# Kernel tuning notes

Hardware: AMD Instinct MI355X
Metric: run time of the kernel (lower is better)

Reference implementation:

```python
import jax, jax.numpy as jnp
import numpy as np

B, IN_DIM, HID, PROJ, OUT = 32768, 4097, 2048, 512, 3
FEAT = IN_DIM - 1
EPS = 1e-12  # F.normalize eps


def setup_inputs() -> dict:
    key = jax.random.key(0)
    ks = jax.random.split(key, 16)
    x_feat = jax.random.normal(ks[0], (B, FEAT), dtype=jnp.float32)
    flag = jax.random.randint(ks[1], (B, 1), 0, 2).astype(jnp.float32)
    x = jnp.concatenate([x_feat, flag], axis=1)  # [B, IN_DIM], last col is 0/1 flag

    def lin(k, fan_in, fan_out):
        bound = 1.0 / np.sqrt(fan_in)
        kw, kb = jax.random.split(k)
        W = jax.random.uniform(kw, (fan_in, fan_out), jnp.float32, -bound, bound)
        b = jax.random.uniform(kb, (fan_out,), jnp.float32, -bound, bound)
        return W, b

    W1n, b1n = lin(ks[2], FEAT, HID)
    W2n, b2n = lin(ks[3], HID, PROJ)
    Wcn, bcn = lin(ks[4], PROJ, OUT)
    W1o, b1o = lin(ks[5], FEAT, HID)
    W2o, b2o = lin(ks[6], HID, PROJ)
    Wco, bco = lin(ks[7], PROJ, OUT)
    return {"x": x, "W1n": W1n, "b1n": b1n, "W2n": W2n, "b2n": b2n,
            "Wcn": Wcn, "bcn": bcn, "W1o": W1o, "b1o": b1o, "W2o": W2o,
            "b2o": b2o, "Wco": Wco, "bco": bco}


def _path(feat, W1, b1, W2, b2):
    # Linear -> ReLU -> Dropout(eval: identity) -> Linear
    h = jax.nn.relu(feat @ W1 + b1)
    return h @ W2 + b2  # [B, PROJ]


def reference(x, W1n, b1n, W2n, b2n, Wcn, bcn, W1o, b1o, W2o, b2o, Wco, bco):
    flag = x[:, -1:] > 0.5          # [B,1] bool; 1 -> natural path
    feat = x[:, :-1]                # [B, FEAT]
    # Dense 2-expert compute + select (same math as gather/scatter routing).
    z_nat = _path(feat, W1n, b1n, W2n, b2n)
    z_oth = _path(feat, W1o, b1o, W2o, b2o)
    z = jnp.where(flag, z_nat, z_oth)                      # [B, PROJ]
    logits_nat = jax.nn.relu(z_nat) @ Wcn + bcn
    logits_oth = jax.nn.relu(z_oth) @ Wco + bco
    logits = jnp.where(flag, logits_nat, logits_oth)       # [B, OUT]
    norm = jnp.linalg.norm(z, axis=1, keepdims=True)
    z_normalized = z / jnp.maximum(norm, EPS)
    return (z_normalized, logits)
```

## Files before the change

kernel.cpp:

```cpp
#include <hip/hip_runtime.h>
#include <hip/hip_bf16.h>

typedef __bf16 bf16_t;
typedef __attribute__((ext_vector_type(8))) __bf16 bf16x8;
typedef __attribute__((ext_vector_type(4))) __bf16 bf16x4;
typedef __attribute__((ext_vector_type(4))) float f32x4;

#define NROWS 32768
#define FEAT  4096
#define INDIM 4097
#define HID   2048
#define PROJ  512
#define NPAD  33024
#define MTILES 258
#define SENT  0xFFFFFFFFu

__device__ __forceinline__ void load_lds16(const bf16_t* g, char* s) {
  __builtin_amdgcn_global_load_lds(
      (__attribute__((address_space(1))) void*)(void*)g,
      (__attribute__((address_space(3))) void*)s, 16, 0, 0);
}

__global__ __launch_bounds__(256) void init_kernel(unsigned* __restrict__ perm,
                                                   int* __restrict__ cnt) {
  int i = blockIdx.x * 256 + threadIdx.x;
  if (i < NPAD) perm[i] = SENT;
  if (i < 4) cnt[i] = 0;
}

__global__ __launch_bounds__(256) void count_kernel(const float* __restrict__ x,
                                                    int* __restrict__ cnt) {
  int i = blockIdx.x * 256 + threadIdx.x;
  if (i >= NROWS) return;
  float f = x[(long)i * INDIM + FEAT];
  if (f > 0.5f) atomicAdd(&cnt[0], 1);
}

__global__ __launch_bounds__(256) void scatter_kernel(const float* __restrict__ x,
                                                      unsigned* __restrict__ perm,
                                                      int* __restrict__ cnt) {
  int i = blockIdx.x * 256 + threadIdx.x;
  if (i >= NROWS) return;
  float f = x[(long)i * INDIM + FEAT];
  int g = (f > 0.5f) ? 0 : 1;
  int pos = atomicAdd(&cnt[1 + g], 1);
  int off_oth = ((cnt[0] + 127) >> 7) << 7;
  int q = (g == 0) ? pos : off_oth + pos;
  perm[q] = (unsigned)i;
}

__global__ __launch_bounds__(256) void convert_x_kernel(const float* __restrict__ x,
                                                        bf16_t* __restrict__ xbf) {
  const int lane = threadIdx.x & 63;
  const long wid = ((long)blockIdx.x * 256 + threadIdx.x) >> 6;
  const long chunk = wid * 512;
  const long row = chunk >> 12;
  const long col = chunk & 4095;
  const float* src = x + row * INDIM + col + lane;
  bf16_t* dst = xbf + chunk + lane;
#pragma unroll
  for (int j = 0; j < 8; ++j)
    dst[j * 64] = (bf16_t)src[j * 64];
}

__global__ __launch_bounds__(256) void transpose_convert_kernel(
    const float* __restrict__ W, bf16_t* __restrict__ Wt, int K, int N) {
  __shared__ float tile[32][33];
  const int n0 = blockIdx.x << 5;
  const int k0 = blockIdx.y << 5;
  const int t = threadIdx.x;
  const int r = t >> 3;
  const int c4 = (t & 7) << 2;
  f32x4 v = *(const f32x4*)(W + (long)(k0 + r) * N + n0 + c4);
#pragma unroll
  for (int i = 0; i < 4; ++i) tile[r][c4 + i] = v[i];
  __syncthreads();
  bf16x4 o;
#pragma unroll
  for (int i = 0; i < 4; ++i) o[i] = (bf16_t)tile[c4 + i][r];
  *(bf16x4*)(Wt + (long)(n0 + r) * K + k0 + c4) = o;
}

template <bool GATHER, bool RELU_BF16>
__global__ __launch_bounds__(256) void gemm_kernel(
    const bf16_t* __restrict__ A,
    const bf16_t* __restrict__ BtNat, const bf16_t* __restrict__ BtOth,
    const float* __restrict__ biasNat, const float* __restrict__ biasOth,
    void* __restrict__ Cout,
    const unsigned* __restrict__ perm, const int* __restrict__ cnt,
    const int K, const int N) {
  __shared__ char smem[16384];
  const int tid = threadIdx.x;
  const int tile_m = blockIdx.y;
  const int qbase = tile_m << 7;
  if (perm[qbase] == SENT) return;
  const int n0 = blockIdx.x << 7;
  const int n_nat = cnt[0];
  const int m_tiles_nat = (n_nat + 127) >> 7;
  const bool nat = (tile_m < m_tiles_nat);
  const bf16_t* __restrict__ Bt = nat ? BtNat : BtOth;
  const float* __restrict__ bias = nat ? biasNat : biasOth;

  const int r0 = tid >> 2;
  const int kc = tid & 3;
  long arow0, arow1;
  if (GATHER) {
    unsigned p0 = perm[qbase + r0];
    unsigned p1 = perm[qbase + r0 + 64];
    arow0 = (p0 == SENT) ? 0 : (long)p0;
    arow1 = (p1 == SENT) ? 0 : (long)p1;
  } else {
    arow0 = qbase + r0;
    arow1 = qbase + r0 + 64;
  }
  const bf16_t* srcA0 = A + arow0 * K + (kc << 3);
  const bf16_t* srcA1 = A + arow1 * K + (kc << 3);
  const bf16_t* srcB0 = Bt + (long)(n0 + r0) * K + (kc << 3);
  const bf16_t* srcB1 = Bt + (long)(n0 + r0 + 64) * K + (kc << 3);

  const int wave = tid >> 6;
  const int lane = tid & 63;
  const int quad = lane >> 4;
  const int l16 = lane & 15;
  const int wm = (wave >> 1) << 6;
  const int wn = (wave & 1) << 6;

  char* const Alds = smem;
  char* const Blds = smem + 8192;
  char* const dstA0 = Alds + (wave << 10);
  char* const dstA1 = Alds + 4096 + (wave << 10);
  char* const dstB0 = Blds + (wave << 10);
  char* const dstB1 = Blds + 4096 + (wave << 10);

  f32x4 acc[4][4] = {};

  const int kiters = K >> 5;
  for (int kt = 0; kt < kiters; ++kt) {
    __syncthreads();
    load_lds16(srcA0, dstA0);
    load_lds16(srcA1, dstA1);
    load_lds16(srcB0, dstB0);
    load_lds16(srcB1, dstB1);
    srcA0 += 32; srcA1 += 32; srcB0 += 32; srcB1 += 32;
    __syncthreads();
    bf16x8 af[4], bfr[4];
#pragma unroll
    for (int i = 0; i < 4; ++i)
      af[i] = *(const bf16x8*)(Alds + (((wm + (i << 4) + l16) << 5) + (quad << 3)) * 2);
#pragma unroll
    for (int i = 0; i < 4; ++i)
      bfr[i] = *(const bf16x8*)(Blds + (((wn + (i << 4) + l16) << 5) + (quad << 3)) * 2);
#pragma unroll
    for (int mi = 0; mi < 4; ++mi)
#pragma unroll
      for (int ni = 0; ni < 4; ++ni)
        acc[mi][ni] = __builtin_amdgcn_mfma_f32_16x16x32_bf16(af[mi], bfr[ni], acc[mi][ni], 0, 0, 0);
  }

  float bv[4];
#pragma unroll
  for (int ni = 0; ni < 4; ++ni) bv[ni] = bias[n0 + wn + (ni << 4) + l16];

#pragma unroll
  for (int mi = 0; mi < 4; ++mi) {
#pragma unroll
    for (int ni = 0; ni < 4; ++ni) {
#pragma unroll
      for (int r = 0; r < 4; ++r) {
        const int m = wm + (mi << 4) + (quad << 2) + r;
        const int col = n0 + wn + (ni << 4) + l16;
        float v = acc[mi][ni][r] + bv[ni];
        if (RELU_BF16) {
          v = fmaxf(v, 0.0f);
          ((bf16_t*)Cout)[(long)(qbase + m) * N + col] = (bf16_t)v;
        } else {
          ((float*)Cout)[(long)(qbase + m) * N + col] = v;
        }
      }
    }
  }
}

__global__ __launch_bounds__(256) void epilogue_kernel(
    const float* __restrict__ z,
    const float* __restrict__ Wc0, const float* __restrict__ bc0,
    const float* __restrict__ Wc1, const float* __restrict__ bc1,
    const unsigned* __restrict__ perm, const int* __restrict__ cnt,
    float* __restrict__ out_z, float* __restrict__ out_logits) {
  __shared__ float WcL[2][PROJ * 3];
  for (int i = threadIdx.x; i < PROJ * 3; i += 256) {
    WcL[0][i] = Wc0[i];
    WcL[1][i] = Wc1[i];
  }
  __syncthreads();
  const int wave = threadIdx.x >> 6;
  const int lane = threadIdx.x & 63;
  const int q = blockIdx.x * 4 + wave;
  const unsigned orig = perm[q];
  if (orig == SENT) return;
  const int n_nat = cnt[0];
  const int off_oth = ((n_nat + 127) >> 7) << 7;
  const int g = (q < off_oth) ? 0 : 1;

  float zv[8];
  float ss = 0.f, l0 = 0.f, l1 = 0.f, l2 = 0.f;
#pragma unroll
  for (int i = 0; i < 8; ++i) {
    const int k = i * 64 + lane;
    float v = z[(long)q * PROJ + k];
    zv[i] = v;
    ss += v * v;
    float r = fmaxf(v, 0.f);
    const float* w = &WcL[g][k * 3];
    l0 += r * w[0];
    l1 += r * w[1];
    l2 += r * w[2];
  }
#pragma unroll
  for (int off = 32; off > 0; off >>= 1) {
    ss += __shfl_xor(ss, off);
    l0 += __shfl_xor(l0, off);
    l1 += __shfl_xor(l1, off);
    l2 += __shfl_xor(l2, off);
  }
  const float inv = 1.f / fmaxf(sqrtf(ss), 1e-12f);
#pragma unroll
  for (int i = 0; i < 8; ++i)
    out_z[(long)orig * PROJ + i * 64 + lane] = zv[i] * inv;
  if (lane == 0) {
    const float* bc = g ? bc1 : bc0;
    out_logits[(long)orig * 3 + 0] = l0 + bc[0];
    out_logits[(long)orig * 3 + 1] = l1 + bc[1];
    out_logits[(long)orig * 3 + 2] = l2 + bc[2];
  }
}

extern "C" void kernel_launch(void* const* d_in, const int* in_sizes, int n_in,
                              void* d_out, int out_size, void* d_ws, size_t ws_size,
                              hipStream_t stream) {
  const float* x   = (const float*)d_in[0];
  const float* W1n = (const float*)d_in[1];
  const float* b1n = (const float*)d_in[2];
  const float* W2n = (const float*)d_in[3];
  const float* b2n = (const float*)d_in[4];
  const float* Wcn = (const float*)d_in[5];
  const float* bcn = (const float*)d_in[6];
  const float* W1o = (const float*)d_in[7];
  const float* b1o = (const float*)d_in[8];
  const float* W2o = (const float*)d_in[9];
  const float* b2o = (const float*)d_in[10];
  const float* Wco = (const float*)d_in[11];
  const float* bco = (const float*)d_in[12];

  char* ws = (char*)d_ws;
  bf16_t* xbf  = (bf16_t*)ws;
  float*  z_ws = (float*)ws;
  size_t off = 268435456;
  bf16_t* W1tn = (bf16_t*)(ws + off); off += (size_t)FEAT * HID * 2;
  bf16_t* W1to = (bf16_t*)(ws + off); off += (size_t)FEAT * HID * 2;
  bf16_t* W2tn = (bf16_t*)(ws + off); off += (size_t)HID * PROJ * 2;
  bf16_t* W2to = (bf16_t*)(ws + off); off += (size_t)HID * PROJ * 2;
  bf16_t* h_ws = (bf16_t*)(ws + off); off += (size_t)NPAD * HID * 2;
  unsigned* perm = (unsigned*)(ws + off); off += (size_t)NPAD * 4;
  int* cnt = (int*)(ws + off);

  float* out_z = (float*)d_out;
  float* out_logits = out_z + (size_t)NROWS * PROJ;

  init_kernel<<<(NPAD + 255) / 256, 256, 0, stream>>>(perm, cnt);
  count_kernel<<<NROWS / 256, 256, 0, stream>>>(x, cnt);
  scatter_kernel<<<NROWS / 256, 256, 0, stream>>>(x, perm, cnt);

  convert_x_kernel<<<(int)(((long)NROWS * FEAT / 512) / 4), 256, 0, stream>>>(x, xbf);
  transpose_convert_kernel<<<dim3(HID / 32, FEAT / 32), 256, 0, stream>>>(W1n, W1tn, FEAT, HID);
  transpose_convert_kernel<<<dim3(HID / 32, FEAT / 32), 256, 0, stream>>>(W1o, W1to, FEAT, HID);
  transpose_convert_kernel<<<dim3(PROJ / 32, HID / 32), 256, 0, stream>>>(W2n, W2tn, HID, PROJ);
  transpose_convert_kernel<<<dim3(PROJ / 32, HID / 32), 256, 0, stream>>>(W2o, W2to, HID, PROJ);

  gemm_kernel<true, true><<<dim3(HID / 128, MTILES), 256, 0, stream>>>(
      xbf, W1tn, W1to, b1n, b1o, (void*)h_ws, perm, cnt, FEAT, HID);

  gemm_kernel<false, false><<<dim3(PROJ / 128, MTILES), 256, 0, stream>>>(
      h_ws, W2tn, W2to, b2n, b2o, (void*)z_ws, perm, cnt, HID, PROJ);

  epilogue_kernel<<<NPAD / 4, 256, 0, stream>>>(
      z_ws, Wcn, bcn, Wco, bco, perm, cnt, out_z, out_logits);
}
```

Before: 2.001 ms.

## Replace 128x128 GEMM with 256x256 double-buffered pipelined MFMA kernel

Replaces the simple 128x128-tile GEMM with a 256x256-tile, 512-thread kernel that uses 128KB of dynamic LDS. It double-buffers global-to-LDS loads with explicit vmcnt waits, XOR-swizzles the LDS layout to avoid bank conflicts, and remaps workgroups across XCDs. Row padding for the expert routing grows to 256 so each M tile maps to a single expert. The aim is higher MFMA utilization and less global traffic per FLOP. The trade-offs are heavy register and LDS pressure plus a hand-written schedule whose correctness depends on the wait counts.

```diff
diff --git a/kernel.cpp b/kernel.cpp
--- a/kernel.cpp
+++ b/kernel.cpp
@@ -12,7 +12,7 @@
 #define HID   2048
 #define PROJ  512
 #define NPAD  33024
-#define MTILES 258
+#define MT256 129
 #define SENT  0xFFFFFFFFu
 
 __device__ __forceinline__ void load_lds16(const bf16_t* g, char* s) {
@@ -44,7 +44,7 @@
   float f = x[(long)i * INDIM + FEAT];
   int g = (f > 0.5f) ? 0 : 1;
   int pos = atomicAdd(&cnt[1 + g], 1);
-  int off_oth = ((cnt[0] + 127) >> 7) << 7;
+  int off_oth = ((cnt[0] + 255) >> 8) << 8;
   int q = (g == 0) ? pos : off_oth + pos;
   perm[q] = (unsigned)i;
 }
@@ -82,103 +82,185 @@
 }
 
 template <bool GATHER, bool RELU_BF16>
-__global__ __launch_bounds__(256) void gemm_kernel(
+__global__ __launch_bounds__(512, 2) void gemm256_kernel(
     const bf16_t* __restrict__ A,
     const bf16_t* __restrict__ BtNat, const bf16_t* __restrict__ BtOth,
     const float* __restrict__ biasNat, const float* __restrict__ biasOth,
     void* __restrict__ Cout,
     const unsigned* __restrict__ perm, const int* __restrict__ cnt,
-    const int K, const int N) {
-  __shared__ char smem[16384];
+    const int K, const int N, const int ntn) {
+  extern __shared__ char smem[];
   const int tid = threadIdx.x;
-  const int tile_m = blockIdx.y;
-  const int qbase = tile_m << 7;
+
+  const int nwg = gridDim.x;
+  const int q8 = nwg >> 3, r8g = nwg & 7;
+  const int xcd = blockIdx.x & 7, lo = blockIdx.x >> 3;
+  const int wg = (xcd < r8g ? xcd * (q8 + 1) : r8g * (q8 + 1) + (xcd - r8g) * q8) + lo;
+  const int tile_m = wg / ntn;
+  const int tile_n = wg - tile_m * ntn;
+  const int qbase = tile_m << 8;
   if (perm[qbase] == SENT) return;
-  const int n0 = blockIdx.x << 7;
-  const int n_nat = cnt[0];
-  const int m_tiles_nat = (n_nat + 127) >> 7;
-  const bool nat = (tile_m < m_tiles_nat);
+  const int n0 = tile_n << 8;
+
+  const int off_oth = ((cnt[0] + 255) >> 8) << 8;
+  const bool nat = qbase < off_oth;
   const bf16_t* __restrict__ Bt = nat ? BtNat : BtOth;
   const float* __restrict__ bias = nat ? biasNat : biasOth;
 
-  const int r0 = tid >> 2;
-  const int kc = tid & 3;
-  long arow0, arow1;
+  const int nkt = K >> 6;
+  const int niter = K >> 7;
+
+  const int r8 = tid >> 3;
+  const int kco = ((tid & 7) ^ (r8 & 7)) << 3;
+  long r00, r01, r10, r11;
   if (GATHER) {
-    unsigned p0 = perm[qbase + r0];
-    unsigned p1 = perm[qbase + r0 + 64];
-    arow0 = (p0 == SENT) ? 0 : (long)p0;
-    arow1 = (p1 == SENT) ? 0 : (long)p1;
+    unsigned p00 = perm[qbase + r8];
+    unsigned p10 = perm[qbase + 64 + r8];
+    unsigned p01 = perm[qbase + 128 + r8];
+    unsigned p11 = perm[qbase + 192 + r8];
+    r00 = (p00 == SENT) ? 0 : (long)p00;
+    r10 = (p10 == SENT) ? 0 : (long)p10;
+    r01 = (p01 == SENT) ? 0 : (long)p01;
+    r11 = (p11 == SENT) ? 0 : (long)p11;
   } else {
-    arow0 = qbase + r0;
-    arow1 = qbase + r0 + 64;
-  }
-  const bf16_t* srcA0 = A + arow0 * K + (kc << 3);
-  const bf16_t* srcA1 = A + arow1 * K + (kc << 3);
-  const bf16_t* srcB0 = Bt + (long)(n0 + r0) * K + (kc << 3);
-  const bf16_t* srcB1 = Bt + (long)(n0 + r0 + 64) * K + (kc << 3);
-
-  const int wave = tid >> 6;
-  const int lane = tid & 63;
-  const int quad = lane >> 4;
-  const int l16 = lane & 15;
-  const int wm = (wave >> 1) << 6;
-  const int wn = (wave & 1) << 6;
-
-  char* const Alds = smem;
-  char* const Blds = smem + 8192;
-  char* const dstA0 = Alds + (wave << 10);
-  char* const dstA1 = Alds + 4096 + (wave << 10);
-  char* const dstB0 = Blds + (wave << 10);
-  char* const dstB1 = Blds + 4096 + (wave << 10);
-
-  f32x4 acc[4][4] = {};
-
-  const int kiters = K >> 5;
-  for (int kt = 0; kt < kiters; ++kt) {
-    __syncthreads();
-    load_lds16(srcA0, dstA0);
-    load_lds16(srcA1, dstA1);
-    load_lds16(srcB0, dstB0);
-    load_lds16(srcB1, dstB1);
-    srcA0 += 32; srcA1 += 32; srcB0 += 32; srcB1 += 32;
-    __syncthreads();
-    bf16x8 af[4], bfr[4];
-#pragma unroll
-    for (int i = 0; i < 4; ++i)
-      af[i] = *(const bf16x8*)(Alds + (((wm + (i << 4) + l16) << 5) + (quad << 3)) * 2);
-#pragma unroll
-    for (int i = 0; i < 4; ++i)
-      bfr[i] = *(const bf16x8*)(Blds + (((wn + (i << 4) + l16) << 5) + (quad << 3)) * 2);
-#pragma unroll
-    for (int mi = 0; mi < 4; ++mi)
-#pragma unroll
-      for (int ni = 0; ni < 4; ++ni)
-        acc[mi][ni] = __builtin_amdgcn_mfma_f32_16x16x32_bf16(af[mi], bfr[ni], acc[mi][ni], 0, 0, 0);
-  }
+    r00 = qbase + r8;       r10 = qbase + 64 + r8;
+    r01 = qbase + 128 + r8; r11 = qbase + 192 + r8;
+  }
+  const bf16_t* aS00 = A + r00 * K + kco;
+  const bf16_t* aS10 = A + r10 * K + kco;
+  const bf16_t* aS01 = A + r01 * K + kco;
+  const bf16_t* aS11 = A + r11 * K + kco;
+
+  const int b0 = tid >> 8;
+  const int r32 = r8 & 31;
+  const bf16_t* bS00 = Bt + (long)(n0 + b0 * 64 + r32) * K + kco;
+  const bf16_t* bS10 = Bt + (long)(n0 + b0 * 64 + 32 + r32) * K + kco;
+  const bf16_t* bS01 = Bt + (long)(n0 + 128 + b0 * 64 + r32) * K + kco;
+  const bf16_t* bS11 = Bt + (long)(n0 + 128 + b0 * 64 + 32 + r32) * K + kco;
+
+  const int wave = tid >> 6, lane = tid & 63;
+  const int wmi = wave >> 2, wni = wave & 3;
+  const int quad = lane >> 4, l16 = lane & 15;
+  const int x7 = l16 & 7;
+  const int rx0 = (quad ^ x7) << 4;
+  const int rx1 = ((quad + 4) ^ x7) << 4;
+  const int aRB = (wmi * 64 + l16) * 128;
+  const int bRB = (wni * 32 + l16) * 128;
+  const int wbase = wave << 10;
+
+#define ADST(buf, h, j) ((buf) * 32768 + (h) * 16384 + (j) * 8192)
+#define BDST(buf, h, j) (65536 + (buf) * 32768 + (h) * 16384 + (j) * 8192)
+#define STG_A(buf, h, kt) do { const long ko = ((kt) < nkt) ? ((long)(kt) << 6) : 0; \
+    load_lds16(aS##h##0 + ko, smem + ADST(buf, h, 0) + wbase); \
+    load_lds16(aS##h##1 + ko, smem + ADST(buf, h, 1) + wbase); } while (0)
+#define STG_B(buf, h, kt) do { const long ko = ((kt) < nkt) ? ((long)(kt) << 6) : 0; \
+    load_lds16(bS##h##0 + ko, smem + BDST(buf, h, 0) + wbase); \
+    load_lds16(bS##h##1 + ko, smem + BDST(buf, h, 1) + wbase); } while (0)
+#define RD_A(buf, mi, ks) af[(mi) & 3][ks] = *(const bf16x8*)(smem + (buf) * 32768 \
+    + ((mi) >> 2) * 16384 + aRB + ((mi) & 3) * 2048 + rx##ks)
+#define RD_B(buf, nf, ks) bfr[nf][ks] = *(const bf16x8*)(smem + 65536 + (buf) * 32768 \
+    + ((nf) >> 1) * 16384 + bRB + ((nf) & 1) * 2048 + rx##ks)
+#define MFMA_PH(m0_, n0_) do { \
+    __builtin_amdgcn_s_setprio(1); \
+    _Pragma("unroll") for (int ks_ = 0; ks_ < 2; ++ks_) \
+    _Pragma("unroll") for (int mi_ = 0; mi_ < 4; ++mi_) \
+    _Pragma("unroll") for (int ni_ = 0; ni_ < 2; ++ni_) \
+      acc[(m0_) + mi_][(n0_) + ni_] = __builtin_amdgcn_mfma_f32_16x16x32_bf16( \
+          af[mi_][ks_], bfr[(n0_) + ni_][ks_], acc[(m0_) + mi_][(n0_) + ni_], 0, 0, 0); \
+    __builtin_amdgcn_s_setprio(0); } while (0)
+#define SBAR do { __builtin_amdgcn_sched_barrier(0); __builtin_amdgcn_s_barrier(); } while (0)
+#define VMC6 asm volatile("s_waitcnt vmcnt(6)" ::: "memory")
+
+  f32x4 acc[8][4] = {};
+  bf16x8 af[4][2], bfr[4][2];
+
+  STG_A(0, 0, 0); STG_B(0, 0, 0); STG_B(0, 1, 0); STG_A(0, 1, 0);
+  STG_A(1, 0, 1); STG_B(1, 0, 1); STG_B(1, 1, 1);
+  VMC6; SBAR;
+
+  for (int t = 0; t < niter; ++t) {
+    const int c = t << 1;
+    RD_A(0, 0, 0); RD_A(0, 0, 1); RD_A(0, 1, 0); RD_A(0, 1, 1);
+    RD_A(0, 2, 0); RD_A(0, 2, 1); RD_A(0, 3, 0); RD_A(0, 3, 1);
+    RD_B(0, 0, 0); RD_B(0, 0, 1); RD_B(0, 1, 0); RD_B(0, 1, 1);
+    STG_A(1, 1, c + 1);
+    SBAR;
+    MFMA_PH(0, 0);
+    SBAR;
+    RD_B(0, 2, 0); RD_B(0, 2, 1); RD_B(0, 3, 0); RD_B(0, 3, 1);
+    STG_A(0, 0, c + 2);
+    SBAR;
+    MFMA_PH(0, 2);
+    SBAR;
+    RD_A(0, 4, 0); RD_A(0, 4, 1); RD_A(0, 5, 0); RD_A(0, 5, 1);
+    RD_A(0, 6, 0); RD_A(0, 6, 1); RD_A(0, 7, 0); RD_A(0, 7, 1);
+    STG_B(0, 0, c + 2);
+    SBAR;
+    MFMA_PH(4, 0);
+    SBAR;
+    STG_B(0, 1, c + 2);
+    SBAR;
+    MFMA_PH(4, 2);
+    VMC6;
+    SBAR;
+    RD_A(1, 0, 0); RD_A(1, 0, 1); RD_A(1, 1, 0); RD_A(1, 1, 1);
+    RD_A(1, 2, 0); RD_A(1, 2, 1); RD_A(1, 3, 0); RD_A(1, 3, 1);
+    RD_B(1, 0, 0); RD_B(1, 0, 1); RD_B(1, 1, 0); RD_B(1, 1, 1);
+    STG_A(0, 1, c + 2);
+    SBAR;
+    MFMA_PH(0, 0);
+    SBAR;
+    RD_B(1, 2, 0); RD_B(1, 2, 1); RD_B(1, 3, 0); RD_B(1, 3, 1);
+    STG_A(1, 0, c + 3);
+    SBAR;
+    MFMA_PH(0, 2);
+    SBAR;
+    RD_A(1, 4, 0); RD_A(1, 4, 1); RD_A(1, 5, 0); RD_A(1, 5, 1);
+    RD_A(1, 6, 0); RD_A(1, 6, 1); RD_A(1, 7, 0); RD_A(1, 7, 1);
+    STG_B(1, 0, c + 3);
+    SBAR;
+    MFMA_PH(4, 0);
+    SBAR;
+    STG_B(1, 1, c + 3);
+    SBAR;
+    MFMA_PH(4, 2);
+    VMC6;
+    SBAR;
+  }
+
+  asm volatile("s_waitcnt vmcnt(0)" ::: "memory");
 
   float bv[4];
 #pragma unroll
-  for (int ni = 0; ni < 4; ++ni) bv[ni] = bias[n0 + wn + (ni << 4) + l16];
-
-#pragma unroll
-  for (int mi = 0; mi < 4; ++mi) {
-#pragma unroll
-    for (int ni = 0; ni < 4; ++ni) {
+  for (int nf = 0; nf < 4; ++nf) bv[nf] = bias[n0 + wni * 64 + nf * 16 + l16];
+
+#pragma unroll
+  for (int mi = 0; mi < 8; ++mi) {
+    const long row0 = (long)(qbase + wmi * 128 + mi * 16 + quad * 4);
+#pragma unroll
+    for (int nf = 0; nf < 4; ++nf) {
+      const int col = n0 + wni * 64 + nf * 16 + l16;
 #pragma unroll
       for (int r = 0; r < 4; ++r) {
-        const int m = wm + (mi << 4) + (quad << 2) + r;
-        const int col = n0 + wn + (ni << 4) + l16;
-        float v = acc[mi][ni][r] + bv[ni];
+        float v = acc[mi][nf][r] + bv[nf];
         if (RELU_BF16) {
           v = fmaxf(v, 0.0f);
-          ((bf16_t*)Cout)[(long)(qbase + m) * N + col] = (bf16_t)v;
+          ((bf16_t*)Cout)[(row0 + r) * N + col] = (bf16_t)v;
         } else {
-          ((float*)Cout)[(long)(qbase + m) * N + col] = v;
+          ((float*)Cout)[(row0 + r) * N + col] = v;
         }
       }
     }
   }
+#undef ADST
+#undef BDST
+#undef STG_A
+#undef STG_B
+#undef RD_A
+#undef RD_B
+#undef MFMA_PH
+#undef SBAR
+#undef VMC6
 }
 
 __global__ __launch_bounds__(256) void epilogue_kernel(
@@ -199,7 +281,7 @@
   const unsigned orig = perm[q];
   if (orig == SENT) return;
   const int n_nat = cnt[0];
-  const int off_oth = ((n_nat + 127) >> 7) << 7;
+  const int off_oth = ((n_nat + 255) >> 8) << 8;
   const int g = (q < off_oth) ? 0 : 1;
 
   float zv[8];
@@ -267,6 +349,17 @@
   float* out_z = (float*)d_out;
   float* out_logits = out_z + (size_t)NROWS * PROJ;
 
+  static bool attr_done = false;
+  if (!attr_done) {
+    auto* k1 = gemm256_kernel<true, true>;
+    auto* k2 = gemm256_kernel<false, false>;
+    (void)hipFuncSetAttribute(reinterpret_cast<const void*>(k1),
+                              hipFuncAttributeMaxDynamicSharedMemorySize, 131072);
+    (void)hipFuncSetAttribute(reinterpret_cast<const void*>(k2),
+                              hipFuncAttributeMaxDynamicSharedMemorySize, 131072);
+    attr_done = true;
+  }
+
   init_kernel<<<(NPAD + 255) / 256, 256, 0, stream>>>(perm, cnt);
   count_kernel<<<NROWS / 256, 256, 0, stream>>>(x, cnt);
   scatter_kernel<<<NROWS / 256, 256, 0, stream>>>(x, perm, cnt);
@@ -277,11 +370,11 @@
   transpose_convert_kernel<<<dim3(PROJ / 32, HID / 32), 256, 0, stream>>>(W2n, W2tn, HID, PROJ);
   transpose_convert_kernel<<<dim3(PROJ / 32, HID / 32), 256, 0, stream>>>(W2o, W2to, HID, PROJ);
 
-  gemm_kernel<true, true><<<dim3(HID / 128, MTILES), 256, 0, stream>>>(
-      xbf, W1tn, W1to, b1n, b1o, (void*)h_ws, perm, cnt, FEAT, HID);
-
-  gemm_kernel<false, false><<<dim3(PROJ / 128, MTILES), 256, 0, stream>>>(
-      h_ws, W2tn, W2to, b2n, b2o, (void*)z_ws, perm, cnt, HID, PROJ);
+  gemm256_kernel<true, true><<<dim3(MT256 * 8), 512, 131072, stream>>>(
+      xbf, W1tn, W1to, b1n, b1o, (void*)h_ws, perm, cnt, FEAT, HID, 8);
+
+  gemm256_kernel<false, false><<<dim3(MT256 * 2), 512, 131072, stream>>>(
+      h_ws, W2tn, W2to, b2n, b2o, (void*)z_ws, perm, cnt, HID, PROJ, 2);
 
   epilogue_kernel<<<NPAD / 4, 256, 0, stream>>>(
       z_ws, Wcn, bcn, Wco, bco, perm, cnt, out_z, out_logits);
```

Measured after the change: 1.726 ms. 1.16x faster.
